# Kernel tuning notes

Measured on AMD Instinct MI355X. Metric: run time of the kernel, lower is better.

The kernel has to match this reference:

```python
import jax, jax.numpy as jnp
import numpy as np

NUM_NODES = 100000
NUM_EDGES = 1600000
NUM_GRAPHS = 64
IN_DIM = 128
HID = 128
OUT_DIM = 256
NUM_LAYERS = 5
BN_EPS = 1e-5


def _bn(t, gamma, beta):
    # BatchNorm1d forward with batch statistics (biased variance), as in train mode
    m = jnp.mean(t, axis=0)
    v = jnp.var(t, axis=0)
    return gamma * (t - m) * jax.lax.rsqrt(v + BN_EPS) + beta


def setup_inputs() -> dict:
    key = jax.random.key(0)
    ks = jax.random.split(key, 16)
    x = jax.random.normal(ks[0], (NUM_NODES, IN_DIM), dtype=jnp.float32)
    edge_index = jax.random.randint(ks[1], (2, NUM_EDGES), 0, NUM_NODES, dtype=jnp.int64)
    batch = jnp.sort(jax.random.randint(ks[2], (NUM_NODES,), 0, NUM_GRAPHS, dtype=jnp.int64))
    s1 = 1.0 / np.sqrt(IN_DIM)
    s2 = 1.0 / np.sqrt(HID)
    # stacked per-layer GIN MLP params: Linear(HID,HID) -> BN -> ReLU -> Linear(HID,HID)
    w1 = jax.random.normal(ks[3], (NUM_LAYERS, HID, HID), dtype=jnp.float32) * s1
    b1 = jnp.zeros((NUM_LAYERS, HID), dtype=jnp.float32)
    gamma1 = jnp.ones((NUM_LAYERS, HID), dtype=jnp.float32)
    beta1 = jnp.zeros((NUM_LAYERS, HID), dtype=jnp.float32)
    w2 = jax.random.normal(ks[4], (NUM_LAYERS, HID, HID), dtype=jnp.float32) * s2
    b2 = jnp.zeros((NUM_LAYERS, HID), dtype=jnp.float32)
    # outer per-layer BatchNorm after each GINConv
    gamma_bn = jnp.ones((NUM_LAYERS, HID), dtype=jnp.float32)
    beta_bn = jnp.zeros((NUM_LAYERS, HID), dtype=jnp.float32)
    # output projection Linear(HID, OUT_DIM)
    wp = jax.random.normal(ks[5], (HID, OUT_DIM), dtype=jnp.float32) * s2
    bp = jnp.zeros((OUT_DIM,), dtype=jnp.float32)
    return {"x": x, "edge_index": edge_index, "batch": batch,
            "w1": w1, "b1": b1, "gamma1": gamma1, "beta1": beta1,
            "w2": w2, "b2": b2, "gamma_bn": gamma_bn, "beta_bn": beta_bn,
            "wp": wp, "bp": bp}


def reference(x, edge_index, batch, w1, b1, gamma1, beta1, w2, b2, gamma_bn, beta_bn, wp, bp):
    src, dst = edge_index[0], edge_index[1]
    h = x
    for i in range(NUM_LAYERS):
        # GINConv, eps=0: mlp((1+eps)*h + sum_{j in N(i)} h_j)
        agg = jax.ops.segment_sum(h[src], dst, num_segments=NUM_NODES)
        z = h + agg
        t = _bn(z @ w1[i] + b1[i], gamma1[i], beta1[i])
        t = jax.nn.relu(t)
        t = t @ w2[i] + b2[i]
        # outer BatchNorm + ReLU (dropout p handled as identity in eval)
        t = jax.nn.relu(_bn(t, gamma_bn[i], beta_bn[i]))
        h = h + t  # residual (dims always match)
    node_emb = h
    # global mean pool per graph
    sums = jax.ops.segment_sum(h, batch, num_segments=NUM_GRAPHS)
    counts = jax.ops.segment_sum(jnp.ones((NUM_NODES,), dtype=h.dtype), batch, num_segments=NUM_GRAPHS)
    pooled = sums / jnp.maximum(counts, 1.0)[:, None]
    graph_emb = pooled @ wp + bp
    return graph_emb, node_emb
```

## Files before the change

kernel.cpp:

```cpp
#include <hip/hip_runtime.h>

#define NNODES 100000
#define NEDGES 1600000
#define NGRAPHS 64
#define HID 128
#define OUTD 256
#define NLAYERS 5
#define BN_EPS 1e-5f
#define NBUCK 196
#define BUCKCAP 9216
#define FILL_BLOCKS 391
#define NREP 8

typedef __attribute__((ext_vector_type(8))) short short8;
typedef __attribute__((ext_vector_type(4))) float f32x4;

__device__ inline unsigned short f2b(float f) {
    union { float f; unsigned int u; } a; a.f = f;
    unsigned int u = a.u;
    return (unsigned short)((u + 0x7FFF + ((u >> 16) & 1)) >> 16);
}
__device__ inline float b2f(unsigned short b) {
    union { unsigned int u; float f; } a; a.u = ((unsigned int)b) << 16;
    return a.f;
}

union U8 { short8 v; unsigned short u[8]; };

__global__ void k_init(const float* __restrict__ x, float* __restrict__ h,
                       ushort* __restrict__ hb,
                       const float* __restrict__ w1, const float* __restrict__ w2,
                       unsigned short* __restrict__ WT) {
    int b = blockIdx.x;
    if (b < 12500) {
        int i = b * 256 + threadIdx.x;
        float4 v = ((const float4*)x)[i];
        ((float4*)h)[i] = v;
        ushort4 o;
        o.x = f2b(v.x); o.y = f2b(v.y); o.z = f2b(v.z); o.w = f2b(v.w);
        ((ushort4*)hb)[i] = o;
    } else {
        int t = (b - 12500) * 256 + threadIdx.x;
        int mat = t >> 14;
        int rem = t & 16383;
        int k = rem >> 7, n = rem & 127;
        const float* src = (mat < 5) ? &w1[(size_t)mat * 16384]
                                     : &w2[(size_t)(mat - 5) * 16384];
        WT[(size_t)mat * 16384 + n * 128 + k] = f2b(src[k * 128 + n]);
    }
}

__global__ void k_bcur0(int* __restrict__ bcur) {
    int t = threadIdx.x;
    if (t < NBUCK) bcur[t] = t * BUCKCAP;
}

__global__ __launch_bounds__(256) void k_fill1(
    const int* __restrict__ srcv, const int* __restrict__ dstv,
    int* __restrict__ bcur, unsigned int* __restrict__ packed) {
    __shared__ int hist[NBUCK];
    __shared__ int base[NBUCK];
    int tid = threadIdx.x;
    int e0 = blockIdx.x * 4096;
    for (int i = tid; i < NBUCK; i += 256) hist[i] = 0;
    __syncthreads();
#pragma unroll
    for (int i = 0; i < 16; i++) {
        int e = e0 + i * 256 + tid;
        if (e < NEDGES) atomicAdd(&hist[dstv[e] >> 9], 1);
    }
    __syncthreads();
    for (int i = tid; i < NBUCK; i += 256) {
        int c = hist[i];
        base[i] = c ? atomicAdd(&bcur[i], c) : 0;
        hist[i] = 0;
    }
    __syncthreads();
#pragma unroll
    for (int i = 0; i < 16; i++) {
        int e = e0 + i * 256 + tid;
        if (e < NEDGES) {
            int d = dstv[e];
            int b = d >> 9;
            int r = atomicAdd(&hist[b], 1);
            packed[base[b] + r] = ((unsigned int)srcv[e] << 9) | (unsigned int)(d & 511);
        }
    }
}

__global__ __launch_bounds__(256) void k_fill2(
    const unsigned int* __restrict__ packed, const int* __restrict__ bcur,
    int2* __restrict__ off2, int* __restrict__ adj) {
    __shared__ int deg[512];
    __shared__ int cur[512];
    int tid = threadIdx.x;
    int b = blockIdx.x;
    int base = b * BUCKCAP;
    int cnt = bcur[b] - base;
    deg[tid] = 0; deg[tid + 256] = 0;
    __syncthreads();
    for (int i = tid; i < cnt; i += 256)
        atomicAdd(&deg[packed[base + i] & 511], 1);
    __syncthreads();
    cur[tid] = deg[tid]; cur[tid + 256] = deg[tid + 256];
    __syncthreads();
    for (int o = 1; o < 512; o <<= 1) {
        int u0 = (tid >= o) ? cur[tid - o] : 0;
        int u1 = (tid + 256 >= o) ? cur[tid + 256 - o] : 0;
        __syncthreads();
        cur[tid] += u0; cur[tid + 256] += u1;
        __syncthreads();
    }
    int nbase = b * 512;
#pragma unroll
    for (int i = 0; i < 2; i++) {
        int t = tid + i * 256;
        int st = base + cur[t] - deg[t];
        int n = nbase + t;
        if (n < NNODES) off2[n] = make_int2(st, st + deg[t]);
    }
    __syncthreads();
#pragma unroll
    for (int i = 0; i < 2; i++) {
        int t = tid + i * 256;
        cur[t] = base + cur[t] - deg[t];
    }
    __syncthreads();
    for (int i = tid; i < cnt; i += 256) {
        unsigned int p = packed[base + i];
        int r = atomicAdd(&cur[p & 511], 1);
        adj[r] = (int)(p >> 9);
    }
}

__global__ __launch_bounds__(256) void k_agg(const ushort* __restrict__ hb,
                                             const int2* __restrict__ off2,
                                             const int* __restrict__ adj,
                                             ushort* __restrict__ zb) {
    int tid = threadIdx.x;
    int node = blockIdx.x * 16 + (tid >> 4);
    int c = tid & 15;
    const short8* hb8 = (const short8*)hb;
    size_t self = (size_t)node * 16 + c;

    U8 sv; sv.v = hb8[self];
    float acc[8];
#pragma unroll
    for (int k = 0; k < 8; k++) acc[k] = b2f(sv.u[k]);

    int2 oo = off2[node];
    int e = oo.x, e1 = oo.y;
    for (; e + 8 <= e1; e += 8) {
        int s[8];
#pragma unroll
        for (int j = 0; j < 8; j++) s[j] = adj[e + j];
        U8 u[8];
#pragma unroll
        for (int j = 0; j < 8; j++) u[j].v = hb8[(size_t)s[j] * 16 + c];
#pragma unroll
        for (int j = 0; j < 8; j++)
#pragma unroll
            for (int k = 0; k < 8; k++) acc[k] += b2f(u[j].u[k]);
    }
    for (; e + 4 <= e1; e += 4) {
        int s0 = adj[e], s1 = adj[e + 1], s2 = adj[e + 2], s3 = adj[e + 3];
        U8 u0, u1, u2, u3;
        u0.v = hb8[(size_t)s0 * 16 + c];
        u1.v = hb8[(size_t)s1 * 16 + c];
        u2.v = hb8[(size_t)s2 * 16 + c];
        u3.v = hb8[(size_t)s3 * 16 + c];
#pragma unroll
        for (int k = 0; k < 8; k++)
            acc[k] += (b2f(u0.u[k]) + b2f(u1.u[k])) + (b2f(u2.u[k]) + b2f(u3.u[k]));
    }
    for (; e < e1; e++) {
        int s = adj[e];
        U8 u; u.v = hb8[(size_t)s * 16 + c];
#pragma unroll
        for (int k = 0; k < 8; k++) acc[k] += b2f(u.u[k]);
    }

    U8 o;
#pragma unroll
    for (int k = 0; k < 8; k++) o.u[k] = f2b(acc[k]);
    ((short8*)zb)[self] = o.v;
}

__global__ __launch_bounds__(256) void k_gemm1(
    const ushort* __restrict__ A, const unsigned short* __restrict__ WT,
    const float* __restrict__ bias, ushort* __restrict__ C,
    float* __restrict__ stats) {
    __shared__ float lstat[256];
    int tid = threadIdx.x;
    int wave = tid >> 6;
    int lane = tid & 63;
    int q = lane >> 4;
    int l16 = lane & 15;
    int rowbase = blockIdx.x * 128 + wave * 32;

    f32x4 acc[2][8];
#pragma unroll
    for (int rt = 0; rt < 2; rt++)
#pragma unroll
        for (int nt = 0; nt < 8; nt++) acc[rt][nt] = (f32x4){0.f, 0.f, 0.f, 0.f};

    for (int kc = 0; kc < 4; kc++) {
        int k0 = kc * 32 + q * 8;
        short8 bf[8];
#pragma unroll
        for (int nt = 0; nt < 8; nt++)
            bf[nt] = *(const short8*)&WT[(size_t)(nt * 16 + l16) * 128 + k0];
#pragma unroll
        for (int rt = 0; rt < 2; rt++) {
            int row = rowbase + rt * 16 + l16;
            if (row >= NNODES) row = NNODES - 1;
            short8 av = *(const short8*)&A[(size_t)row * 128 + k0];
#pragma unroll
            for (int nt = 0; nt < 8; nt++)
                acc[rt][nt] = __builtin_amdgcn_mfma_f32_16x16x32_bf16(
                    av, bf[nt], acc[rt][nt], 0, 0, 0);
        }
    }

    lstat[tid] = 0.f;
    __syncthreads();
#pragma unroll
    for (int nt = 0; nt < 8; nt++) {
        float b = bias[nt * 16 + l16];
        float csum = 0.f, csq = 0.f;
#pragma unroll
        for (int rt = 0; rt < 2; rt++) {
            int rb = rowbase + rt * 16 + q * 4;
#pragma unroll
            for (int r = 0; r < 4; r++) {
                int row = rb + r;
                if (row < NNODES) {
                    float v = acc[rt][nt][r] + b;
                    C[(size_t)row * 128 + nt * 16 + l16] = f2b(v);
                    csum += v; csq += v * v;
                }
            }
        }
        csum += __shfl_xor(csum, 16, 64); csq += __shfl_xor(csq, 16, 64);
        csum += __shfl_xor(csum, 32, 64); csq += __shfl_xor(csq, 32, 64);
        if (q == 0) {
            atomicAdd(&lstat[nt * 16 + l16], csum);
            atomicAdd(&lstat[128 + nt * 16 + l16], csq);
        }
    }
    __syncthreads();
    atomicAdd(&stats[((blockIdx.x & (NREP - 1)) << 8) + tid], lstat[tid]);
}

__global__ __launch_bounds__(256) void k_gemm2(
    const ushort* __restrict__ A, const unsigned short* __restrict__ WT,
    const float* __restrict__ bias, ushort* __restrict__ C,
    const float* __restrict__ statsIn, const float* __restrict__ gamma,
    const float* __restrict__ beta, float* __restrict__ stats) {
    __shared__ float lstat[256];
    __shared__ float s_sc[128], s_sh[128];
    int tid = threadIdx.x;
    if (tid < 128) {
        float s = 0.f, qq = 0.f;
#pragma unroll
        for (int r = 0; r < NREP; r++) {
            s  += statsIn[r * 256 + tid];
            qq += statsIn[r * 256 + 128 + tid];
        }
        float m = s * (1.f / NNODES);
        float var = qq * (1.f / NNODES) - m * m;
        float sc = gamma[tid] * rsqrtf(var + BN_EPS);
        s_sc[tid] = sc;
        s_sh[tid] = beta[tid] - m * sc;
    }
    __syncthreads();

    int wave = tid >> 6;
    int lane = tid & 63;
    int q = lane >> 4;
    int l16 = lane & 15;
    int rowbase = blockIdx.x * 128 + wave * 32;

    f32x4 acc[2][8];
#pragma unroll
    for (int rt = 0; rt < 2; rt++)
#pragma unroll
        for (int nt = 0; nt < 8; nt++) acc[rt][nt] = (f32x4){0.f, 0.f, 0.f, 0.f};

    for (int kc = 0; kc < 4; kc++) {
        int k0 = kc * 32 + q * 8;
        short8 bf[8];
#pragma unroll
        for (int nt = 0; nt < 8; nt++)
            bf[nt] = *(const short8*)&WT[(size_t)(nt * 16 + l16) * 128 + k0];

        float4 s0 = *(const float4*)&s_sc[k0];
        float4 s1 = *(const float4*)&s_sc[k0 + 4];
        float4 t0 = *(const float4*)&s_sh[k0];
        float4 t1 = *(const float4*)&s_sh[k0 + 4];
        float scl[8] = {s0.x, s0.y, s0.z, s0.w, s1.x, s1.y, s1.z, s1.w};
        float shf[8] = {t0.x, t0.y, t0.z, t0.w, t1.x, t1.y, t1.z, t1.w};
#pragma unroll
        for (int rt = 0; rt < 2; rt++) {
            int row = rowbase + rt * 16 + l16;
            if (row >= NNODES) row = NNODES - 1;
            union { short8 s; unsigned short u[8]; } in, cv;
            in.s = *(const short8*)&A[(size_t)row * 128 + k0];
#pragma unroll
            for (int j = 0; j < 8; j++) {
                float f = fmaxf(b2f(in.u[j]) * scl[j] + shf[j], 0.f);
                cv.u[j] = f2b(f);
            }
#pragma unroll
            for (int nt = 0; nt < 8; nt++)
                acc[rt][nt] = __builtin_amdgcn_mfma_f32_16x16x32_bf16(
                    cv.s, bf[nt], acc[rt][nt], 0, 0, 0);
        }
    }

    lstat[tid] = 0.f;
    __syncthreads();
#pragma unroll
    for (int nt = 0; nt < 8; nt++) {
        float b = bias[nt * 16 + l16];
        float csum = 0.f, csq = 0.f;
#pragma unroll
        for (int rt = 0; rt < 2; rt++) {
            int rb = rowbase + rt * 16 + q * 4;
#pragma unroll
            for (int r = 0; r < 4; r++) {
                int row = rb + r;
                if (row < NNODES) {
                    float v = acc[rt][nt][r] + b;
                    C[(size_t)row * 128 + nt * 16 + l16] = f2b(v);
                    csum += v; csq += v * v;
                }
            }
        }
        csum += __shfl_xor(csum, 16, 64); csq += __shfl_xor(csq, 16, 64);
        csum += __shfl_xor(csum, 32, 64); csq += __shfl_xor(csq, 32, 64);
        if (q == 0) {
            atomicAdd(&lstat[nt * 16 + l16], csum);
            atomicAdd(&lstat[128 + nt * 16 + l16], csq);
        }
    }
    __syncthreads();
    atomicAdd(&stats[((blockIdx.x & (NREP - 1)) << 8) + tid], lstat[tid]);
}

__global__ void k_resid(float* __restrict__ h, ushort* __restrict__ hb,
                        const ushort* __restrict__ t2b,
                        const float* __restrict__ statsIn,
                        const float* __restrict__ gamma, const float* __restrict__ beta) {
    __shared__ float s_sc[128], s_sh[128];
    int tid = threadIdx.x;
    if (tid < 128) {
        float s = 0.f, qq = 0.f;
#pragma unroll
        for (int r = 0; r < NREP; r++) {
            s  += statsIn[r * 256 + tid];
            qq += statsIn[r * 256 + 128 + tid];
        }
        float m = s * (1.f / NNODES);
        float var = qq * (1.f / NNODES) - m * m;
        float sc = gamma[tid] * rsqrtf(var + BN_EPS);
        s_sc[tid] = sc;
        s_sh[tid] = beta[tid] - m * sc;
    }
    __syncthreads();
    int i = blockIdx.x * 256 + tid;
    int c4 = (i & 31) * 4;
    float4 sc = *(const float4*)&s_sc[c4];
    float4 sh = *(const float4*)&s_sh[c4];
    ushort4 t = ((const ushort4*)t2b)[i];
    float4 hv = ((float4*)h)[i];
    hv.x += fmaxf(b2f(t.x) * sc.x + sh.x, 0.f);
    hv.y += fmaxf(b2f(t.y) * sc.y + sh.y, 0.f);
    hv.z += fmaxf(b2f(t.z) * sc.z + sh.z, 0.f);
    hv.w += fmaxf(b2f(t.w) * sc.w + sh.w, 0.f);
    ((float4*)h)[i] = hv;
    ushort4 o;
    o.x = f2b(hv.x); o.y = f2b(hv.y); o.z = f2b(hv.z); o.w = f2b(hv.w);
    ((ushort4*)hb)[i] = o;
}

__global__ void k_pool(const float* __restrict__ h, const int* __restrict__ batch,
                       float* __restrict__ pooled, float* __restrict__ gcnt) {
    __shared__ float4 red[256];
    __shared__ int lcnt[NGRAPHS];
    int t = threadIdx.x;
    int d4 = t & 31, sub = t >> 5;
    int n0 = blockIdx.x * 128;
    if (n0 >= NNODES) return;
    int n1 = n0 + 128; if (n1 > NNODES) n1 = NNODES;
    if (t < NGRAPHS) lcnt[t] = 0;
    __syncthreads();
    if (t < n1 - n0) atomicAdd(&lcnt[batch[n0 + t]], 1);
    __syncthreads();
    if (t < NGRAPHS && lcnt[t]) atomicAdd(&gcnt[t], (float)lcnt[t]);

    int glo = batch[n0], ghi = batch[n1 - 1];
    for (int g = glo; g <= ghi; g++) {
        float4 acc = make_float4(0.f, 0.f, 0.f, 0.f);
        for (int r = n0 + sub; r < n1; r += 8) {
            if (batch[r] == g) {
                float4 v = ((const float4*)h)[(size_t)r * 32 + d4];
                acc.x += v.x; acc.y += v.y; acc.z += v.z; acc.w += v.w;
            }
        }
        red[t] = acc;
        __syncthreads();
        if (sub < 4) {
            float4 o = red[t + 128];
            red[t].x += o.x; red[t].y += o.y; red[t].z += o.z; red[t].w += o.w;
        }
        __syncthreads();
        if (sub < 2) {
            float4 o = red[t + 64];
            red[t].x += o.x; red[t].y += o.y; red[t].z += o.z; red[t].w += o.w;
        }
        __syncthreads();
        if (sub == 0) {
            float4 o = red[t + 32];
            float4 a = red[t];
            a.x += o.x; a.y += o.y; a.z += o.z; a.w += o.w;
            atomicAdd(&pooled[g * 128 + d4 * 4 + 0], a.x);
            atomicAdd(&pooled[g * 128 + d4 * 4 + 1], a.y);
            atomicAdd(&pooled[g * 128 + d4 * 4 + 2], a.z);
            atomicAdd(&pooled[g * 128 + d4 * 4 + 3], a.w);
        }
        __syncthreads();
    }
}

__global__ void k_proj(const float* __restrict__ pooled, const float* __restrict__ cnt,
                       const float* __restrict__ wp, const float* __restrict__ bp,
                       float* __restrict__ out) {
    __shared__ float prow[128];
    int g = blockIdx.x, c = threadIdx.x;
    if (c < 128) prow[c] = pooled[g * 128 + c] / fmaxf(cnt[g], 1.f);
    __syncthreads();
    float acc = bp[c];
    for (int k = 0; k < 128; k++) acc += prow[k] * wp[k * 256 + c];
    out[g * 256 + c] = acc;
}

extern "C" void kernel_launch(void* const* d_in, const int* in_sizes, int n_in,
                              void* d_out, int out_size, void* d_ws, size_t ws_size,
                              hipStream_t stream) {
    const float* x    = (const float*)d_in[0];
    const int*   eidx = (const int*)d_in[1];
    const int*   batch= (const int*)d_in[2];
    const float* w1   = (const float*)d_in[3];
    const float* b1   = (const float*)d_in[4];
    const float* g1   = (const float*)d_in[5];
    const float* be1  = (const float*)d_in[6];
    const float* w2   = (const float*)d_in[7];
    const float* b2   = (const float*)d_in[8];
    const float* gbn  = (const float*)d_in[9];
    const float* bbn  = (const float*)d_in[10];
    const float* wp   = (const float*)d_in[11];
    const float* bp   = (const float*)d_in[12];

    float* out  = (float*)d_out;
    float* gemb = out;
    float* h    = out + (size_t)NGRAPHS * OUTD;

    char* w = (char*)d_ws;
    ushort* hb   = (ushort*)w; w += (size_t)NNODES * 128 * 2;
    ushort* zb   = (ushort*)w; w += (size_t)NNODES * 128 * 2;
    ushort* tb   = (ushort*)w; w += (size_t)NNODES * 128 * 2;
    int2*  off2  = (int2*)w;  w += (size_t)NNODES * 8;
    int*   adj   = (int*)w;   w += (size_t)NBUCK * BUCKCAP * 4;
    unsigned short* WT = (unsigned short*)w; w += (size_t)10 * 16384 * 2;
    int*   bcur  = (int*)w;   w += 256 * 4;
    float* statsAll = (float*)w; w += (size_t)10 * NREP * 256 * 4;
    float* pooled= (float*)w; w += (size_t)NGRAPHS * HID * 4;
    float* gcnt  = (float*)w; w += NGRAPHS * 4;

    ushort* t2b = zb;
    unsigned int* packed = (unsigned int*)tb;

    const int* srcv = eidx;
    const int* dstv = eidx + NEDGES;

    k_init<<<12500 + 640, 256, 0, stream>>>(x, h, hb, w1, w2, WT);

    hipMemsetAsync(statsAll, 0,
                   ((size_t)10 * NREP * 256 + NGRAPHS * HID + NGRAPHS) * 4, stream);

    k_bcur0<<<1, 256, 0, stream>>>(bcur);
    k_fill1<<<FILL_BLOCKS, 256, 0, stream>>>(srcv, dstv, bcur, packed);
    k_fill2<<<NBUCK, 256, 0, stream>>>(packed, bcur, off2, adj);

    const int GB = (NNODES + 127) / 128;
    for (int i = 0; i < NLAYERS; i++) {
        float* st1 = statsAll + (size_t)(2 * i) * NREP * 256;
        float* st2 = statsAll + (size_t)(2 * i + 1) * NREP * 256;
        k_agg<<<NNODES / 16, 256, 0, stream>>>(hb, off2, adj, zb);
        k_gemm1<<<GB, 256, 0, stream>>>(
            zb, WT + (size_t)i * 16384, b1 + i * HID, tb, st1);
        k_gemm2<<<GB, 256, 0, stream>>>(
            tb, WT + (size_t)(5 + i) * 16384, b2 + i * HID, t2b,
            st1, g1 + i * HID, be1 + i * HID, st2);
        k_resid<<<NNODES * 128 / 4 / 256, 256, 0, stream>>>(
            h, hb, t2b, st2, gbn + i * HID, bbn + i * HID);
    }

    k_pool<<<(NNODES + 127) / 128, 256, 0, stream>>>(h, batch, pooled, gcnt);
    k_proj<<<NGRAPHS, 256, 0, stream>>>(pooled, gcnt, wp, bp, gemb);
}
```

Baseline: 1.050 ms.

## Store bf16 node features column-sliced so each XCD gathers one L2-resident slice

The bf16 feature buffers move from row-major to 8 column slices of 16 features each, and k_init, k_agg, k_gemm1 and k_resid are rewritten to read and write that layout. The aggregation grid puts the slice index in the low 3 bits of blockIdx, so with round-robin dispatch each XCD should gather from a single slice of about 3.2 MB. That slice could stay in its L2 instead of spilling the full 25.6 MB table. The trade-off is that each gather is now a 32-byte segment per node rather than a full row, and edge offsets and indices are read 8 times per layer. The bcur initialisation is also folded into k_init, which removes one kernel launch.

```diff
diff --git a/kernel.cpp b/kernel.cpp
--- a/kernel.cpp
+++ b/kernel.cpp
@@ -11,6 +11,7 @@
 #define BUCKCAP 9216
 #define FILL_BLOCKS 391
 #define NREP 8
+#define NCHUNK 782
 
 typedef __attribute__((ext_vector_type(8))) short short8;
 typedef __attribute__((ext_vector_type(4))) float f32x4;
@@ -27,32 +28,35 @@
 
 union U8 { short8 v; unsigned short u[8]; };
 
+
 __global__ void k_init(const float* __restrict__ x, float* __restrict__ h,
-                       ushort* __restrict__ hb,
+                       ushort* __restrict__ hb_cb,
                        const float* __restrict__ w1, const float* __restrict__ w2,
-                       unsigned short* __restrict__ WT) {
+                       unsigned short* __restrict__ WT, int* __restrict__ bcur) {
     int b = blockIdx.x;
-    if (b < 12500) {
-        int i = b * 256 + threadIdx.x;
-        float4 v = ((const float4*)x)[i];
-        ((float4*)h)[i] = v;
-        ushort4 o;
-        o.x = f2b(v.x); o.y = f2b(v.y); o.z = f2b(v.z); o.w = f2b(v.w);
-        ((ushort4*)hb)[i] = o;
+    if (b < 6250) {
+        int i8 = b * 256 + threadIdx.x;
+        float4 v0 = ((const float4*)x)[i8 * 2];
+        float4 v1 = ((const float4*)x)[i8 * 2 + 1];
+        ((float4*)h)[i8 * 2] = v0;
+        ((float4*)h)[i8 * 2 + 1] = v1;
+        int node = i8 >> 4, c = i8 & 15;
+        int slice = c >> 1, half = c & 1;
+        U8 o;
+        o.u[0] = f2b(v0.x); o.u[1] = f2b(v0.y); o.u[2] = f2b(v0.z); o.u[3] = f2b(v0.w);
+        o.u[4] = f2b(v1.x); o.u[5] = f2b(v1.y); o.u[6] = f2b(v1.z); o.u[7] = f2b(v1.w);
+        ((short8*)hb_cb)[(size_t)slice * NNODES * 2 + (size_t)node * 2 + half] = o.v;
     } else {
-        int t = (b - 12500) * 256 + threadIdx.x;
+        int t = (b - 6250) * 256 + threadIdx.x;
         int mat = t >> 14;
         int rem = t & 16383;
         int k = rem >> 7, n = rem & 127;
         const float* src = (mat < 5) ? &w1[(size_t)mat * 16384]
                                      : &w2[(size_t)(mat - 5) * 16384];
         WT[(size_t)mat * 16384 + n * 128 + k] = f2b(src[k * 128 + n]);
-    }
-}
-
-__global__ void k_bcur0(int* __restrict__ bcur) {
-    int t = threadIdx.x;
-    if (t < NBUCK) bcur[t] = t * BUCKCAP;
+        if (b == 6250 && threadIdx.x < NBUCK)
+            bcur[threadIdx.x] = threadIdx.x * BUCKCAP;
+    }
 }
 
 __global__ __launch_bounds__(256) void k_fill1(
@@ -133,30 +137,34 @@
     }
 }
 
-__global__ __launch_bounds__(256) void k_agg(const ushort* __restrict__ hb,
+__global__ __launch_bounds__(256) void k_agg(const ushort* __restrict__ hb_cb,
                                              const int2* __restrict__ off2,
                                              const int* __restrict__ adj,
-                                             ushort* __restrict__ zb) {
+                                             ushort* __restrict__ zb_cb) {
     int tid = threadIdx.x;
-    int node = blockIdx.x * 16 + (tid >> 4);
-    int c = tid & 15;
-    const short8* hb8 = (const short8*)hb;
-    size_t self = (size_t)node * 16 + c;
-
-    U8 sv; sv.v = hb8[self];
+    int s = blockIdx.x & 7;
+    int chunk = blockIdx.x >> 3;
+    int nl = tid >> 1;
+    int half = tid & 1;
+    int node = chunk * 128 + nl;
+    int nodec = (node < NNODES) ? node : (NNODES - 1);
+    const short8* src = (const short8*)hb_cb + (size_t)s * NNODES * 2;
+    size_t selfidx = (size_t)nodec * 2 + half;
+
+    U8 sv; sv.v = src[selfidx];
     float acc[8];
 #pragma unroll
     for (int k = 0; k < 8; k++) acc[k] = b2f(sv.u[k]);
 
-    int2 oo = off2[node];
+    int2 oo = off2[nodec];
     int e = oo.x, e1 = oo.y;
     for (; e + 8 <= e1; e += 8) {
-        int s[8];
-#pragma unroll
-        for (int j = 0; j < 8; j++) s[j] = adj[e + j];
+        int sj[8];
+#pragma unroll
+        for (int j = 0; j < 8; j++) sj[j] = adj[e + j];
         U8 u[8];
 #pragma unroll
-        for (int j = 0; j < 8; j++) u[j].v = hb8[(size_t)s[j] * 16 + c];
+        for (int j = 0; j < 8; j++) u[j].v = src[(size_t)sj[j] * 2 + half];
 #pragma unroll
         for (int j = 0; j < 8; j++)
 #pragma unroll
@@ -165,25 +173,27 @@
     for (; e + 4 <= e1; e += 4) {
         int s0 = adj[e], s1 = adj[e + 1], s2 = adj[e + 2], s3 = adj[e + 3];
         U8 u0, u1, u2, u3;
-        u0.v = hb8[(size_t)s0 * 16 + c];
-        u1.v = hb8[(size_t)s1 * 16 + c];
-        u2.v = hb8[(size_t)s2 * 16 + c];
-        u3.v = hb8[(size_t)s3 * 16 + c];
+        u0.v = src[(size_t)s0 * 2 + half];
+        u1.v = src[(size_t)s1 * 2 + half];
+        u2.v = src[(size_t)s2 * 2 + half];
+        u3.v = src[(size_t)s3 * 2 + half];
 #pragma unroll
         for (int k = 0; k < 8; k++)
             acc[k] += (b2f(u0.u[k]) + b2f(u1.u[k])) + (b2f(u2.u[k]) + b2f(u3.u[k]));
     }
     for (; e < e1; e++) {
-        int s = adj[e];
-        U8 u; u.v = hb8[(size_t)s * 16 + c];
+        int sj = adj[e];
+        U8 u; u.v = src[(size_t)sj * 2 + half];
 #pragma unroll
         for (int k = 0; k < 8; k++) acc[k] += b2f(u.u[k]);
     }
 
-    U8 o;
-#pragma unroll
-    for (int k = 0; k < 8; k++) o.u[k] = f2b(acc[k]);
-    ((short8*)zb)[self] = o.v;
+    if (node < NNODES) {
+        U8 o;
+#pragma unroll
+        for (int k = 0; k < 8; k++) o.u[k] = f2b(acc[k]);
+        ((short8*)zb_cb)[(size_t)s * NNODES * 2 + (size_t)node * 2 + half] = o.v;
+    }
 }
 
 __global__ __launch_bounds__(256) void k_gemm1(
@@ -204,17 +214,19 @@
 #pragma unroll
         for (int nt = 0; nt < 8; nt++) acc[rt][nt] = (f32x4){0.f, 0.f, 0.f, 0.f};
 
+    const short8* A8 = (const short8*)A;
     for (int kc = 0; kc < 4; kc++) {
         int k0 = kc * 32 + q * 8;
         short8 bf[8];
 #pragma unroll
         for (int nt = 0; nt < 8; nt++)
             bf[nt] = *(const short8*)&WT[(size_t)(nt * 16 + l16) * 128 + k0];
+        size_t sbase = (size_t)(kc * 2 + (q >> 1)) * NNODES * 2 + (q & 1);
 #pragma unroll
         for (int rt = 0; rt < 2; rt++) {
             int row = rowbase + rt * 16 + l16;
             if (row >= NNODES) row = NNODES - 1;
-            short8 av = *(const short8*)&A[(size_t)row * 128 + k0];
+            short8 av = A8[sbase + (size_t)row * 2];
 #pragma unroll
             for (int nt = 0; nt < 8; nt++)
                 acc[rt][nt] = __builtin_amdgcn_mfma_f32_16x16x32_bf16(
@@ -348,10 +360,10 @@
     atomicAdd(&stats[((blockIdx.x & (NREP - 1)) << 8) + tid], lstat[tid]);
 }
 
-__global__ void k_resid(float* __restrict__ h, ushort* __restrict__ hb,
-                        const ushort* __restrict__ t2b,
-                        const float* __restrict__ statsIn,
-                        const float* __restrict__ gamma, const float* __restrict__ beta) {
+__global__ __launch_bounds__(256) void k_resid(
+    float* __restrict__ h, ushort* __restrict__ hb_cb,
+    const ushort* __restrict__ t2b, const float* __restrict__ statsIn,
+    const float* __restrict__ gamma, const float* __restrict__ beta) {
     __shared__ float s_sc[128], s_sh[128];
     int tid = threadIdx.x;
     if (tid < 128) {
@@ -368,20 +380,32 @@
         s_sh[tid] = beta[tid] - m * sc;
     }
     __syncthreads();
-    int i = blockIdx.x * 256 + tid;
-    int c4 = (i & 31) * 4;
-    float4 sc = *(const float4*)&s_sc[c4];
-    float4 sh = *(const float4*)&s_sh[c4];
-    ushort4 t = ((const ushort4*)t2b)[i];
-    float4 hv = ((float4*)h)[i];
-    hv.x += fmaxf(b2f(t.x) * sc.x + sh.x, 0.f);
-    hv.y += fmaxf(b2f(t.y) * sc.y + sh.y, 0.f);
-    hv.z += fmaxf(b2f(t.z) * sc.z + sh.z, 0.f);
-    hv.w += fmaxf(b2f(t.w) * sc.w + sh.w, 0.f);
-    ((float4*)h)[i] = hv;
-    ushort4 o;
-    o.x = f2b(hv.x); o.y = f2b(hv.y); o.z = f2b(hv.z); o.w = f2b(hv.w);
-    ((ushort4*)hb)[i] = o;
+    int s = tid >> 5;
+    int j = tid & 31;
+    int node = blockIdx.x * 16 + (j >> 1);
+    int half = j & 1;
+    int col0 = s * 16 + half * 8;
+    U8 t; t.v = *(const short8*)&t2b[(size_t)node * 128 + col0];
+    float4 h0 = *(const float4*)&h[(size_t)node * 128 + col0];
+    float4 h1 = *(const float4*)&h[(size_t)node * 128 + col0 + 4];
+    float4 sc0 = *(const float4*)&s_sc[col0];
+    float4 sc1 = *(const float4*)&s_sc[col0 + 4];
+    float4 sh0 = *(const float4*)&s_sh[col0];
+    float4 sh1 = *(const float4*)&s_sh[col0 + 4];
+    h0.x += fmaxf(b2f(t.u[0]) * sc0.x + sh0.x, 0.f);
+    h0.y += fmaxf(b2f(t.u[1]) * sc0.y + sh0.y, 0.f);
+    h0.z += fmaxf(b2f(t.u[2]) * sc0.z + sh0.z, 0.f);
+    h0.w += fmaxf(b2f(t.u[3]) * sc0.w + sh0.w, 0.f);
+    h1.x += fmaxf(b2f(t.u[4]) * sc1.x + sh1.x, 0.f);
+    h1.y += fmaxf(b2f(t.u[5]) * sc1.y + sh1.y, 0.f);
+    h1.z += fmaxf(b2f(t.u[6]) * sc1.z + sh1.z, 0.f);
+    h1.w += fmaxf(b2f(t.u[7]) * sc1.w + sh1.w, 0.f);
+    *(float4*)&h[(size_t)node * 128 + col0] = h0;
+    *(float4*)&h[(size_t)node * 128 + col0 + 4] = h1;
+    U8 o;
+    o.u[0] = f2b(h0.x); o.u[1] = f2b(h0.y); o.u[2] = f2b(h0.z); o.u[3] = f2b(h0.w);
+    o.u[4] = f2b(h1.x); o.u[5] = f2b(h1.y); o.u[6] = f2b(h1.z); o.u[7] = f2b(h1.w);
+    ((short8*)hb_cb)[(size_t)s * NNODES * 2 + (size_t)node * 2 + half] = o.v;
 }
 
 __global__ void k_pool(const float* __restrict__ h, const int* __restrict__ batch,
@@ -484,12 +508,11 @@
     const int* srcv = eidx;
     const int* dstv = eidx + NEDGES;
 
-    k_init<<<12500 + 640, 256, 0, stream>>>(x, h, hb, w1, w2, WT);
+    k_init<<<6250 + 640, 256, 0, stream>>>(x, h, hb, w1, w2, WT, bcur);
 
     hipMemsetAsync(statsAll, 0,
                    ((size_t)10 * NREP * 256 + NGRAPHS * HID + NGRAPHS) * 4, stream);
 
-    k_bcur0<<<1, 256, 0, stream>>>(bcur);
     k_fill1<<<FILL_BLOCKS, 256, 0, stream>>>(srcv, dstv, bcur, packed);
     k_fill2<<<NBUCK, 256, 0, stream>>>(packed, bcur, off2, adj);
 
@@ -497,13 +520,13 @@
     for (int i = 0; i < NLAYERS; i++) {
         float* st1 = statsAll + (size_t)(2 * i) * NREP * 256;
         float* st2 = statsAll + (size_t)(2 * i + 1) * NREP * 256;
-        k_agg<<<NNODES / 16, 256, 0, stream>>>(hb, off2, adj, zb);
+        k_agg<<<8 * NCHUNK, 256, 0, stream>>>(hb, off2, adj, zb);
         k_gemm1<<<GB, 256, 0, stream>>>(
             zb, WT + (size_t)i * 16384, b1 + i * HID, tb, st1);
         k_gemm2<<<GB, 256, 0, stream>>>(
             tb, WT + (size_t)(5 + i) * 16384, b2 + i * HID, t2b,
             st1, g1 + i * HID, be1 + i * HID, st2);
-        k_resid<<<NNODES * 128 / 4 / 256, 256, 0, stream>>>(
+        k_resid<<<NNODES / 16, 256, 0, stream>>>(
             h, hb, t2b, st2, gbn + i * HID, bbn + i * HID);
     }
 
```

Result: slower. 1.137 ms (+8.3%).

## Fuse neighbor aggregation into first GEMM via swizzled shared-memory tile

Applied to the files above, without the earlier changes.

Merges the sparse aggregation kernel with the first MLP GEMM. Each block aggregates 64 nodes into a bank-swizzled LDS tile, then runs the bf16 MFMA GEMM plus BN statistics straight from shared memory. This removes the zb global write and read-back and one launch per layer. It also folds the bucket-cursor init into k_init, dropping one more launch. In exchange, the GEMM tile shrinks to 64 rows per block and LDS use rises, which may lower occupancy and reload weights more often.

```diff
diff --git a/kernel.cpp b/kernel.cpp
--- a/kernel.cpp
+++ b/kernel.cpp
@@ -11,6 +11,7 @@
 #define BUCKCAP 9216
 #define FILL_BLOCKS 391
 #define NREP 8
+#define AG1B 1563
 
 typedef __attribute__((ext_vector_type(8))) short short8;
 typedef __attribute__((ext_vector_type(4))) float f32x4;
@@ -30,7 +31,7 @@
 __global__ void k_init(const float* __restrict__ x, float* __restrict__ h,
                        ushort* __restrict__ hb,
                        const float* __restrict__ w1, const float* __restrict__ w2,
-                       unsigned short* __restrict__ WT) {
+                       unsigned short* __restrict__ WT, int* __restrict__ bcur) {
     int b = blockIdx.x;
     if (b < 12500) {
         int i = b * 256 + threadIdx.x;
@@ -47,12 +48,9 @@
         const float* src = (mat < 5) ? &w1[(size_t)mat * 16384]
                                      : &w2[(size_t)(mat - 5) * 16384];
         WT[(size_t)mat * 16384 + n * 128 + k] = f2b(src[k * 128 + n]);
-    }
-}
-
-__global__ void k_bcur0(int* __restrict__ bcur) {
-    int t = threadIdx.x;
-    if (t < NBUCK) bcur[t] = t * BUCKCAP;
+        if (b == 12500 && threadIdx.x < NBUCK)
+            bcur[threadIdx.x] = threadIdx.x * BUCKCAP;
+    }
 }
 
 __global__ __launch_bounds__(256) void k_fill1(
@@ -133,76 +131,74 @@
     }
 }
 
-__global__ __launch_bounds__(256) void k_agg(const ushort* __restrict__ hb,
-                                             const int2* __restrict__ off2,
-                                             const int* __restrict__ adj,
-                                             ushort* __restrict__ zb) {
-    int tid = threadIdx.x;
-    int node = blockIdx.x * 16 + (tid >> 4);
-    int c = tid & 15;
-    const short8* hb8 = (const short8*)hb;
-    size_t self = (size_t)node * 16 + c;
-
-    U8 sv; sv.v = hb8[self];
-    float acc[8];
-#pragma unroll
-    for (int k = 0; k < 8; k++) acc[k] = b2f(sv.u[k]);
-
-    int2 oo = off2[node];
-    int e = oo.x, e1 = oo.y;
-    for (; e + 8 <= e1; e += 8) {
-        int s[8];
-#pragma unroll
-        for (int j = 0; j < 8; j++) s[j] = adj[e + j];
-        U8 u[8];
-#pragma unroll
-        for (int j = 0; j < 8; j++) u[j].v = hb8[(size_t)s[j] * 16 + c];
-#pragma unroll
-        for (int j = 0; j < 8; j++)
-#pragma unroll
-            for (int k = 0; k < 8; k++) acc[k] += b2f(u[j].u[k]);
-    }
-    for (; e + 4 <= e1; e += 4) {
-        int s0 = adj[e], s1 = adj[e + 1], s2 = adj[e + 2], s3 = adj[e + 3];
-        U8 u0, u1, u2, u3;
-        u0.v = hb8[(size_t)s0 * 16 + c];
-        u1.v = hb8[(size_t)s1 * 16 + c];
-        u2.v = hb8[(size_t)s2 * 16 + c];
-        u3.v = hb8[(size_t)s3 * 16 + c];
-#pragma unroll
-        for (int k = 0; k < 8; k++)
-            acc[k] += (b2f(u0.u[k]) + b2f(u1.u[k])) + (b2f(u2.u[k]) + b2f(u3.u[k]));
-    }
-    for (; e < e1; e++) {
-        int s = adj[e];
-        U8 u; u.v = hb8[(size_t)s * 16 + c];
-#pragma unroll
-        for (int k = 0; k < 8; k++) acc[k] += b2f(u.u[k]);
-    }
-
-    U8 o;
-#pragma unroll
-    for (int k = 0; k < 8; k++) o.u[k] = f2b(acc[k]);
-    ((short8*)zb)[self] = o.v;
-}
-
-__global__ __launch_bounds__(256) void k_gemm1(
-    const ushort* __restrict__ A, const unsigned short* __restrict__ WT,
+__global__ __launch_bounds__(256) void k_ag1(
+    const ushort* __restrict__ hb, const int2* __restrict__ off2,
+    const int* __restrict__ adj, const unsigned short* __restrict__ WT,
     const float* __restrict__ bias, ushort* __restrict__ C,
     float* __restrict__ stats) {
+    __shared__ ushort zt[64 * 128];
     __shared__ float lstat[256];
     int tid = threadIdx.x;
+    int grp = tid >> 4;
+    int d4 = tid & 15;
+    const short8* hb8 = (const short8*)hb;
+
+    for (int pass = 0; pass < 4; pass++) {
+        int rl = pass * 16 + grp;
+        int node = blockIdx.x * 64 + rl;
+        int nodec = (node < NNODES) ? node : (NNODES - 1);
+        U8 sv; sv.v = hb8[(size_t)nodec * 16 + d4];
+        float acc[8];
+#pragma unroll
+        for (int k = 0; k < 8; k++) acc[k] = b2f(sv.u[k]);
+        int2 oo = off2[nodec];
+        int e = oo.x, e1 = oo.y;
+        for (; e + 8 <= e1; e += 8) {
+            int sj[8];
+#pragma unroll
+            for (int j = 0; j < 8; j++) sj[j] = adj[e + j];
+            U8 u[8];
+#pragma unroll
+            for (int j = 0; j < 8; j++) u[j].v = hb8[(size_t)sj[j] * 16 + d4];
+#pragma unroll
+            for (int j = 0; j < 8; j++)
+#pragma unroll
+                for (int k = 0; k < 8; k++) acc[k] += b2f(u[j].u[k]);
+        }
+        for (; e + 4 <= e1; e += 4) {
+            int s0 = adj[e], s1 = adj[e + 1], s2 = adj[e + 2], s3 = adj[e + 3];
+            U8 u0, u1, u2, u3;
+            u0.v = hb8[(size_t)s0 * 16 + d4];
+            u1.v = hb8[(size_t)s1 * 16 + d4];
+            u2.v = hb8[(size_t)s2 * 16 + d4];
+            u3.v = hb8[(size_t)s3 * 16 + d4];
+#pragma unroll
+            for (int k = 0; k < 8; k++)
+                acc[k] += (b2f(u0.u[k]) + b2f(u1.u[k])) + (b2f(u2.u[k]) + b2f(u3.u[k]));
+        }
+        for (; e < e1; e++) {
+            int sj = adj[e];
+            U8 u; u.v = hb8[(size_t)sj * 16 + d4];
+#pragma unroll
+            for (int k = 0; k < 8; k++) acc[k] += b2f(u.u[k]);
+        }
+        U8 o;
+#pragma unroll
+        for (int k = 0; k < 8; k++) o.u[k] = f2b(acc[k]);
+        *(short8*)((char*)zt + ((rl * 256 + d4 * 16) ^ ((rl & 7) << 4))) = o.v;
+    }
+    __syncthreads();
+
     int wave = tid >> 6;
     int lane = tid & 63;
     int q = lane >> 4;
     int l16 = lane & 15;
-    int rowbase = blockIdx.x * 128 + wave * 32;
-
-    f32x4 acc[2][8];
-#pragma unroll
-    for (int rt = 0; rt < 2; rt++)
-#pragma unroll
-        for (int nt = 0; nt < 8; nt++) acc[rt][nt] = (f32x4){0.f, 0.f, 0.f, 0.f};
+    int rowbase = blockIdx.x * 64 + wave * 16;
+    int rl = wave * 16 + l16;
+
+    f32x4 acc2[8];
+#pragma unroll
+    for (int nt = 0; nt < 8; nt++) acc2[nt] = (f32x4){0.f, 0.f, 0.f, 0.f};
 
     for (int kc = 0; kc < 4; kc++) {
         int k0 = kc * 32 + q * 8;
@@ -210,16 +206,12 @@
 #pragma unroll
         for (int nt = 0; nt < 8; nt++)
             bf[nt] = *(const short8*)&WT[(size_t)(nt * 16 + l16) * 128 + k0];
-#pragma unroll
-        for (int rt = 0; rt < 2; rt++) {
-            int row = rowbase + rt * 16 + l16;
-            if (row >= NNODES) row = NNODES - 1;
-            short8 av = *(const short8*)&A[(size_t)row * 128 + k0];
-#pragma unroll
-            for (int nt = 0; nt < 8; nt++)
-                acc[rt][nt] = __builtin_amdgcn_mfma_f32_16x16x32_bf16(
-                    av, bf[nt], acc[rt][nt], 0, 0, 0);
-        }
+        short8 av = *(const short8*)(
+            (char*)zt + ((rl * 256 + k0 * 2) ^ ((rl & 7) << 4)));
+#pragma unroll
+        for (int nt = 0; nt < 8; nt++)
+            acc2[nt] = __builtin_amdgcn_mfma_f32_16x16x32_bf16(
+                av, bf[nt], acc2[nt], 0, 0, 0);
     }
 
     lstat[tid] = 0.f;
@@ -228,17 +220,14 @@
     for (int nt = 0; nt < 8; nt++) {
         float b = bias[nt * 16 + l16];
         float csum = 0.f, csq = 0.f;
-#pragma unroll
-        for (int rt = 0; rt < 2; rt++) {
-            int rb = rowbase + rt * 16 + q * 4;
-#pragma unroll
-            for (int r = 0; r < 4; r++) {
-                int row = rb + r;
-                if (row < NNODES) {
-                    float v = acc[rt][nt][r] + b;
-                    C[(size_t)row * 128 + nt * 16 + l16] = f2b(v);
-                    csum += v; csq += v * v;
-                }
+        int rb = rowbase + q * 4;
+#pragma unroll
+        for (int r = 0; r < 4; r++) {
+            int row = rb + r;
+            if (row < NNODES) {
+                float v = acc2[nt][r] + b;
+                C[(size_t)row * 128 + nt * 16 + l16] = f2b(v);
+                csum += v; csq += v * v;
             }
         }
         csum += __shfl_xor(csum, 16, 64); csq += __shfl_xor(csq, 16, 64);
@@ -468,7 +457,7 @@
 
     char* w = (char*)d_ws;
     ushort* hb   = (ushort*)w; w += (size_t)NNODES * 128 * 2;
-    ushort* zb   = (ushort*)w; w += (size_t)NNODES * 128 * 2;
+    ushort* t2b  = (ushort*)w; w += (size_t)NNODES * 128 * 2;
     ushort* tb   = (ushort*)w; w += (size_t)NNODES * 128 * 2;
     int2*  off2  = (int2*)w;  w += (size_t)NNODES * 8;
     int*   adj   = (int*)w;   w += (size_t)NBUCK * BUCKCAP * 4;
@@ -478,29 +467,25 @@
     float* pooled= (float*)w; w += (size_t)NGRAPHS * HID * 4;
     float* gcnt  = (float*)w; w += NGRAPHS * 4;
 
-    ushort* t2b = zb;
     unsigned int* packed = (unsigned int*)tb;
 
     const int* srcv = eidx;
     const int* dstv = eidx + NEDGES;
 
-    k_init<<<12500 + 640, 256, 0, stream>>>(x, h, hb, w1, w2, WT);
+    k_init<<<12500 + 640, 256, 0, stream>>>(x, h, hb, w1, w2, WT, bcur);
 
     hipMemsetAsync(statsAll, 0,
                    ((size_t)10 * NREP * 256 + NGRAPHS * HID + NGRAPHS) * 4, stream);
 
-    k_bcur0<<<1, 256, 0, stream>>>(bcur);
     k_fill1<<<FILL_BLOCKS, 256, 0, stream>>>(srcv, dstv, bcur, packed);
     k_fill2<<<NBUCK, 256, 0, stream>>>(packed, bcur, off2, adj);
 
-    const int GB = (NNODES + 127) / 128;
     for (int i = 0; i < NLAYERS; i++) {
         float* st1 = statsAll + (size_t)(2 * i) * NREP * 256;
         float* st2 = statsAll + (size_t)(2 * i + 1) * NREP * 256;
-        k_agg<<<NNODES / 16, 256, 0, stream>>>(hb, off2, adj, zb);
-        k_gemm1<<<GB, 256, 0, stream>>>(
-            zb, WT + (size_t)i * 16384, b1 + i * HID, tb, st1);
-        k_gemm2<<<GB, 256, 0, stream>>>(
+        k_ag1<<<AG1B, 256, 0, stream>>>(
+            hb, off2, adj, WT + (size_t)i * 16384, b1 + i * HID, tb, st1);
+        k_gemm2<<<(NNODES + 127) / 128, 256, 0, stream>>>(
             tb, WT + (size_t)(5 + i) * 16384, b2 + i * HID, t2b,
             st1, g1 + i * HID, be1 + i * HID, st2);
         k_resid<<<NNODES * 128 / 4 / 256, 256, 0, stream>>>(
```

Result: slower. 1.116 ms (+6.3%).

## Halve GEMM row tiles, widen stats replicas, batch resid work, fold bcur init

Applied to the files above, without the earlier changes.

The two GEMM kernels now give each block 64 rows (16 per wave) instead of 128, so the grid doubles to 1563 blocks and each wave holds half as many accumulators. The BN-statistics atomic replicas go from 8 to 16 to spread contention from the larger block count. The residual kernel now handles four float4 elements per thread with a quarter of the blocks. The separate bucket-cursor init kernel is folded into k_init to save a launch. In exchange, each WT B-fragment load is reused across half as many rows, so weight reloads per output row double.

```diff
diff --git a/kernel.cpp b/kernel.cpp
--- a/kernel.cpp
+++ b/kernel.cpp
@@ -10,7 +10,8 @@
 #define NBUCK 196
 #define BUCKCAP 9216
 #define FILL_BLOCKS 391
-#define NREP 8
+#define NREP 16
+#define GB64 1563
 
 typedef __attribute__((ext_vector_type(8))) short short8;
 typedef __attribute__((ext_vector_type(4))) float f32x4;
@@ -30,7 +31,7 @@
 __global__ void k_init(const float* __restrict__ x, float* __restrict__ h,
                        ushort* __restrict__ hb,
                        const float* __restrict__ w1, const float* __restrict__ w2,
-                       unsigned short* __restrict__ WT) {
+                       unsigned short* __restrict__ WT, int* __restrict__ bcur) {
     int b = blockIdx.x;
     if (b < 12500) {
         int i = b * 256 + threadIdx.x;
@@ -47,12 +48,9 @@
         const float* src = (mat < 5) ? &w1[(size_t)mat * 16384]
                                      : &w2[(size_t)(mat - 5) * 16384];
         WT[(size_t)mat * 16384 + n * 128 + k] = f2b(src[k * 128 + n]);
-    }
-}
-
-__global__ void k_bcur0(int* __restrict__ bcur) {
-    int t = threadIdx.x;
-    if (t < NBUCK) bcur[t] = t * BUCKCAP;
+        if (b == 12500 && threadIdx.x < NBUCK)
+            bcur[threadIdx.x] = threadIdx.x * BUCKCAP;
+    }
 }
 
 __global__ __launch_bounds__(256) void k_fill1(
@@ -196,13 +194,11 @@
     int lane = tid & 63;
     int q = lane >> 4;
     int l16 = lane & 15;
-    int rowbase = blockIdx.x * 128 + wave * 32;
-
-    f32x4 acc[2][8];
-#pragma unroll
-    for (int rt = 0; rt < 2; rt++)
-#pragma unroll
-        for (int nt = 0; nt < 8; nt++) acc[rt][nt] = (f32x4){0.f, 0.f, 0.f, 0.f};
+    int rowbase = blockIdx.x * 64 + wave * 16;
+
+    f32x4 acc[8];
+#pragma unroll
+    for (int nt = 0; nt < 8; nt++) acc[nt] = (f32x4){0.f, 0.f, 0.f, 0.f};
 
     for (int kc = 0; kc < 4; kc++) {
         int k0 = kc * 32 + q * 8;
@@ -210,16 +206,13 @@
 #pragma unroll
         for (int nt = 0; nt < 8; nt++)
             bf[nt] = *(const short8*)&WT[(size_t)(nt * 16 + l16) * 128 + k0];
-#pragma unroll
-        for (int rt = 0; rt < 2; rt++) {
-            int row = rowbase + rt * 16 + l16;
-            if (row >= NNODES) row = NNODES - 1;
-            short8 av = *(const short8*)&A[(size_t)row * 128 + k0];
-#pragma unroll
-            for (int nt = 0; nt < 8; nt++)
-                acc[rt][nt] = __builtin_amdgcn_mfma_f32_16x16x32_bf16(
-                    av, bf[nt], acc[rt][nt], 0, 0, 0);
-        }
+        int row = rowbase + l16;
+        if (row >= NNODES) row = NNODES - 1;
+        short8 av = *(const short8*)&A[(size_t)row * 128 + k0];
+#pragma unroll
+        for (int nt = 0; nt < 8; nt++)
+            acc[nt] = __builtin_amdgcn_mfma_f32_16x16x32_bf16(
+                av, bf[nt], acc[nt], 0, 0, 0);
     }
 
     lstat[tid] = 0.f;
@@ -228,17 +221,14 @@
     for (int nt = 0; nt < 8; nt++) {
         float b = bias[nt * 16 + l16];
         float csum = 0.f, csq = 0.f;
-#pragma unroll
-        for (int rt = 0; rt < 2; rt++) {
-            int rb = rowbase + rt * 16 + q * 4;
-#pragma unroll
-            for (int r = 0; r < 4; r++) {
-                int row = rb + r;
-                if (row < NNODES) {
-                    float v = acc[rt][nt][r] + b;
-                    C[(size_t)row * 128 + nt * 16 + l16] = f2b(v);
-                    csum += v; csq += v * v;
-                }
+        int rb = rowbase + q * 4;
+#pragma unroll
+        for (int r = 0; r < 4; r++) {
+            int row = rb + r;
+            if (row < NNODES) {
+                float v = acc[nt][r] + b;
+                C[(size_t)row * 128 + nt * 16 + l16] = f2b(v);
+                csum += v; csq += v * v;
             }
         }
         csum += __shfl_xor(csum, 16, 64); csq += __shfl_xor(csq, 16, 64);
@@ -279,13 +269,11 @@
     int lane = tid & 63;
     int q = lane >> 4;
     int l16 = lane & 15;
-    int rowbase = blockIdx.x * 128 + wave * 32;
-
-    f32x4 acc[2][8];
-#pragma unroll
-    for (int rt = 0; rt < 2; rt++)
-#pragma unroll
-        for (int nt = 0; nt < 8; nt++) acc[rt][nt] = (f32x4){0.f, 0.f, 0.f, 0.f};
+    int rowbase = blockIdx.x * 64 + wave * 16;
+
+    f32x4 acc[8];
+#pragma unroll
+    for (int nt = 0; nt < 8; nt++) acc[nt] = (f32x4){0.f, 0.f, 0.f, 0.f};
 
     for (int kc = 0; kc < 4; kc++) {
         int k0 = kc * 32 + q * 8;
@@ -300,22 +288,19 @@
         float4 t1 = *(const float4*)&s_sh[k0 + 4];
         float scl[8] = {s0.x, s0.y, s0.z, s0.w, s1.x, s1.y, s1.z, s1.w};
         float shf[8] = {t0.x, t0.y, t0.z, t0.w, t1.x, t1.y, t1.z, t1.w};
-#pragma unroll
-        for (int rt = 0; rt < 2; rt++) {
-            int row = rowbase + rt * 16 + l16;
-            if (row >= NNODES) row = NNODES - 1;
-            union { short8 s; unsigned short u[8]; } in, cv;
-            in.s = *(const short8*)&A[(size_t)row * 128 + k0];
-#pragma unroll
-            for (int j = 0; j < 8; j++) {
-                float f = fmaxf(b2f(in.u[j]) * scl[j] + shf[j], 0.f);
-                cv.u[j] = f2b(f);
-            }
-#pragma unroll
-            for (int nt = 0; nt < 8; nt++)
-                acc[rt][nt] = __builtin_amdgcn_mfma_f32_16x16x32_bf16(
-                    cv.s, bf[nt], acc[rt][nt], 0, 0, 0);
-        }
+        int row = rowbase + l16;
+        if (row >= NNODES) row = NNODES - 1;
+        union { short8 s; unsigned short u[8]; } in, cv;
+        in.s = *(const short8*)&A[(size_t)row * 128 + k0];
+#pragma unroll
+        for (int j = 0; j < 8; j++) {
+            float f = fmaxf(b2f(in.u[j]) * scl[j] + shf[j], 0.f);
+            cv.u[j] = f2b(f);
+        }
+#pragma unroll
+        for (int nt = 0; nt < 8; nt++)
+            acc[nt] = __builtin_amdgcn_mfma_f32_16x16x32_bf16(
+                cv.s, bf[nt], acc[nt], 0, 0, 0);
     }
 
     lstat[tid] = 0.f;
@@ -324,17 +309,14 @@
     for (int nt = 0; nt < 8; nt++) {
         float b = bias[nt * 16 + l16];
         float csum = 0.f, csq = 0.f;
-#pragma unroll
-        for (int rt = 0; rt < 2; rt++) {
-            int rb = rowbase + rt * 16 + q * 4;
-#pragma unroll
-            for (int r = 0; r < 4; r++) {
-                int row = rb + r;
-                if (row < NNODES) {
-                    float v = acc[rt][nt][r] + b;
-                    C[(size_t)row * 128 + nt * 16 + l16] = f2b(v);
-                    csum += v; csq += v * v;
-                }
+        int rb = rowbase + q * 4;
+#pragma unroll
+        for (int r = 0; r < 4; r++) {
+            int row = rb + r;
+            if (row < NNODES) {
+                float v = acc[nt][r] + b;
+                C[(size_t)row * 128 + nt * 16 + l16] = f2b(v);
+                csum += v; csq += v * v;
             }
         }
         csum += __shfl_xor(csum, 16, 64); csq += __shfl_xor(csq, 16, 64);
@@ -348,10 +330,10 @@
     atomicAdd(&stats[((blockIdx.x & (NREP - 1)) << 8) + tid], lstat[tid]);
 }
 
-__global__ void k_resid(float* __restrict__ h, ushort* __restrict__ hb,
-                        const ushort* __restrict__ t2b,
-                        const float* __restrict__ statsIn,
-                        const float* __restrict__ gamma, const float* __restrict__ beta) {
+__global__ __launch_bounds__(256) void k_resid(
+    float* __restrict__ h, ushort* __restrict__ hb,
+    const ushort* __restrict__ t2b, const float* __restrict__ statsIn,
+    const float* __restrict__ gamma, const float* __restrict__ beta) {
     __shared__ float s_sc[128], s_sh[128];
     int tid = threadIdx.x;
     if (tid < 128) {
@@ -368,20 +350,23 @@
         s_sh[tid] = beta[tid] - m * sc;
     }
     __syncthreads();
-    int i = blockIdx.x * 256 + tid;
-    int c4 = (i & 31) * 4;
-    float4 sc = *(const float4*)&s_sc[c4];
-    float4 sh = *(const float4*)&s_sh[c4];
-    ushort4 t = ((const ushort4*)t2b)[i];
-    float4 hv = ((float4*)h)[i];
-    hv.x += fmaxf(b2f(t.x) * sc.x + sh.x, 0.f);
-    hv.y += fmaxf(b2f(t.y) * sc.y + sh.y, 0.f);
-    hv.z += fmaxf(b2f(t.z) * sc.z + sh.z, 0.f);
-    hv.w += fmaxf(b2f(t.w) * sc.w + sh.w, 0.f);
-    ((float4*)h)[i] = hv;
-    ushort4 o;
-    o.x = f2b(hv.x); o.y = f2b(hv.y); o.z = f2b(hv.z); o.w = f2b(hv.w);
-    ((ushort4*)hb)[i] = o;
+#pragma unroll
+    for (int it = 0; it < 4; it++) {
+        int i = blockIdx.x * 1024 + it * 256 + tid;
+        int c4 = (i & 31) * 4;
+        float4 sc = *(const float4*)&s_sc[c4];
+        float4 sh = *(const float4*)&s_sh[c4];
+        ushort4 t = ((const ushort4*)t2b)[i];
+        float4 hv = ((float4*)h)[i];
+        hv.x += fmaxf(b2f(t.x) * sc.x + sh.x, 0.f);
+        hv.y += fmaxf(b2f(t.y) * sc.y + sh.y, 0.f);
+        hv.z += fmaxf(b2f(t.z) * sc.z + sh.z, 0.f);
+        hv.w += fmaxf(b2f(t.w) * sc.w + sh.w, 0.f);
+        ((float4*)h)[i] = hv;
+        ushort4 o;
+        o.x = f2b(hv.x); o.y = f2b(hv.y); o.z = f2b(hv.z); o.w = f2b(hv.w);
+        ((ushort4*)hb)[i] = o;
+    }
 }
 
 __global__ void k_pool(const float* __restrict__ h, const int* __restrict__ batch,
@@ -484,26 +469,24 @@
     const int* srcv = eidx;
     const int* dstv = eidx + NEDGES;
 
-    k_init<<<12500 + 640, 256, 0, stream>>>(x, h, hb, w1, w2, WT);
+    k_init<<<12500 + 640, 256, 0, stream>>>(x, h, hb, w1, w2, WT, bcur);
 
     hipMemsetAsync(statsAll, 0,
                    ((size_t)10 * NREP * 256 + NGRAPHS * HID + NGRAPHS) * 4, stream);
 
-    k_bcur0<<<1, 256, 0, stream>>>(bcur);
     k_fill1<<<FILL_BLOCKS, 256, 0, stream>>>(srcv, dstv, bcur, packed);
     k_fill2<<<NBUCK, 256, 0, stream>>>(packed, bcur, off2, adj);
 
-    const int GB = (NNODES + 127) / 128;
     for (int i = 0; i < NLAYERS; i++) {
         float* st1 = statsAll + (size_t)(2 * i) * NREP * 256;
         float* st2 = statsAll + (size_t)(2 * i + 1) * NREP * 256;
         k_agg<<<NNODES / 16, 256, 0, stream>>>(hb, off2, adj, zb);
-        k_gemm1<<<GB, 256, 0, stream>>>(
+        k_gemm1<<<GB64, 256, 0, stream>>>(
             zb, WT + (size_t)i * 16384, b1 + i * HID, tb, st1);
-        k_gemm2<<<GB, 256, 0, stream>>>(
+        k_gemm2<<<GB64, 256, 0, stream>>>(
             tb, WT + (size_t)(5 + i) * 16384, b2 + i * HID, t2b,
             st1, g1 + i * HID, be1 + i * HID, st2);
-        k_resid<<<NNODES * 128 / 4 / 256, 256, 0, stream>>>(
+        k_resid<<<NNODES * 128 / 4 / 1024, 256, 0, stream>>>(
             h, hb, t2b, st2, gbn + i * HID, bbn + i * HID);
     }
 
```

Result: slower. 1.077 ms (+2.6%).
